# Optimization experiments

Measured on AMD Instinct MI355X. Metric: run time of the kernel, lower is better.

## Reference

```python
import jax, jax.numpy as jnp
import numpy as np

NUM_HEADS = 20


def _rope(t, pos):
    """Rotary embedding (ESM style, rotate_half on full head_dim).
    t: (T, h, d), pos: (T,) float32 position within each sequence."""
    d = t.shape[-1]
    inv_freq = 1.0 / (10000.0 ** (jnp.arange(0, d, 2, dtype=jnp.float32) / d))  # (d/2,)
    freqs = pos[:, None] * inv_freq[None, :]          # (T, d/2)
    emb = jnp.concatenate([freqs, freqs], axis=-1)    # (T, d)
    cos = jnp.cos(emb)[:, None, :]                    # (T, 1, d)
    sin = jnp.sin(emb)[:, None, :]
    x1, x2 = jnp.split(t, 2, axis=-1)
    rot = jnp.concatenate([-x2, x1], axis=-1)
    return t * cos + rot * sin


def setup_inputs() -> dict:
    key = jax.random.key(0)
    ks = jax.random.split(key, 8)
    E = 1280
    lengths = np.array([512, 768, 1024, 1024, 1024, 1280, 1280, 1280], dtype=np.int64)
    cu_lens = jnp.asarray(np.concatenate([[0], np.cumsum(lengths)]).astype(np.int32))
    T = int(lengths.sum())  # 8192
    s = (2.0 / (E + E)) ** 0.5  # xavier-ish scale
    return {
        "x": jax.random.normal(ks[0], (T, E), jnp.float32),
        "cu_lens": cu_lens,
        "max_len": 1280,
        "Wq": jax.random.normal(ks[1], (E, E), jnp.float32) * s,
        "bq": jnp.zeros((E,), jnp.float32),
        "Wk": jax.random.normal(ks[2], (E, E), jnp.float32) * s,
        "bk": jnp.zeros((E,), jnp.float32),
        "Wv": jax.random.normal(ks[3], (E, E), jnp.float32) * s,
        "bv": jnp.zeros((E,), jnp.float32),
        "Wo": jax.random.normal(ks[4], (E, E), jnp.float32) * (2.0 ** 0.5) * s,
        "bo": jnp.zeros((E,), jnp.float32),
    }


def reference(x, cu_lens, max_len, Wq, bq, Wk, bk, Wv, bv, Wo, bo):
    T, E = x.shape
    h = NUM_HEADS
    d = E // h
    scale = d ** -0.5
    # fused QKV projections (q pre-scaled, softmax_scale=1 as in the original)
    q = ((x @ Wq.T + bq) * scale).reshape(T, h, d)
    k = (x @ Wk.T + bk).reshape(T, h, d)
    v = (x @ Wv.T + bv).reshape(T, h, d)
    # per-token sequence id and within-sequence position from cu_lens
    t_idx = jnp.arange(T)
    seq_id = jnp.searchsorted(cu_lens, t_idx, side='right') - 1  # (T,)
    pos = t_idx - cu_lens[seq_id]                                # (T,) int
    # rotary on q and k with per-sequence positions
    posf = pos.astype(jnp.float32)
    q = _rope(q, posf)
    k = _rope(k, posf)
    # scatter packed tokens into padded (B, max_len, h, d) layout
    B = cu_lens.shape[0] - 1
    qp = jnp.zeros((B, max_len, h, d), q.dtype).at[seq_id, pos].set(q)
    kp = jnp.zeros((B, max_len, h, d), k.dtype).at[seq_id, pos].set(k)
    vp = jnp.zeros((B, max_len, h, d), v.dtype).at[seq_id, pos].set(v)
    valid = jnp.zeros((B, max_len), bool).at[seq_id, pos].set(True)
    # non-causal attention within each sequence (block-diagonal over packed tokens)
    scores = jnp.einsum('blhd,bmhd->bhlm', qp, kp)
    scores = jnp.where(valid[:, None, None, :], scores, -1e9)
    attn = jax.nn.softmax(scores, axis=-1)
    o = jnp.einsum('bhlm,bmhd->blhd', attn, vp)
    # gather back to packed layout and apply output projection
    out_tok = o[seq_id, pos].reshape(T, E)
    return out_tok @ Wo.T + bo
```

## Files before the change

kernel.cpp:

```cpp
#include <hip/hip_runtime.h>
#include <hip/hip_bf16.h>
#include <cstdint>

#define E_DIM   1280
#define NHEADS  20
#define HDIM    64
#define QKV_LD  3840

typedef __attribute__((ext_vector_type(8))) short bf8_t;
typedef __attribute__((ext_vector_type(4))) short bf4_t;
typedef __attribute__((ext_vector_type(4))) float f4_t;

__device__ __forceinline__ short f2bs(float f) {
    union { __hip_bfloat16 h; short s; } u;
    u.h = __float2bfloat16(f);
    return u.s;
}

__device__ __forceinline__ f4_t mfma16x32(bf8_t a, bf8_t b, f4_t c) {
    return __builtin_amdgcn_mfma_f32_16x16x32_bf16(a, b, c, 0, 0, 0);
}
__device__ __forceinline__ f4_t mfma16x16(bf4_t a, bf4_t b, f4_t c) {
    return __builtin_amdgcn_mfma_f32_16x16x16bf16_1k(a, b, c, 0, 0, 0);
}

__device__ __forceinline__ void gl_lds16(const void* g, void* l) {
    auto gp = reinterpret_cast<__attribute__((address_space(1))) unsigned int*>(
        reinterpret_cast<uintptr_t>(g));
    auto lp = reinterpret_cast<__attribute__((address_space(3))) unsigned int*>(
        reinterpret_cast<uintptr_t>(l));
    __builtin_amdgcn_global_load_lds(gp, lp, 16, 0, 0);
}

#define QSCALE 0.18033688011112042f

__device__ __forceinline__ void cvt8(__hip_bfloat16* dst, const float* src, float sc) {
    float4 a = *(const float4*)src;
    float4 b = *(const float4*)(src + 4);
    bf8_t v;
    v[0] = f2bs(a.x * sc); v[1] = f2bs(a.y * sc); v[2] = f2bs(a.z * sc); v[3] = f2bs(a.w * sc);
    v[4] = f2bs(b.x * sc); v[5] = f2bs(b.y * sc); v[6] = f2bs(b.z * sc); v[7] = f2bs(b.w * sc);
    *(bf8_t*)dst = v;
}

__global__ __launch_bounds__(256) void prep_kernel(
    const float* __restrict__ x,
    const float* __restrict__ wq, const float* __restrict__ wk,
    const float* __restrict__ wv, const float* __restrict__ wo,
    const float* __restrict__ bq, const float* __restrict__ bk, const float* __restrict__ bv,
    __hip_bfloat16* __restrict__ xbf, __hip_bfloat16* __restrict__ wqkv,
    __hip_bfloat16* __restrict__ wobf, float* __restrict__ bqkv,
    long nx8, long nw8, long nb8)
{
    long u = (long)blockIdx.x * 256 + threadIdx.x;
    if (u < nx8) { cvt8(xbf + u * 8, x + u * 8, 1.0f); return; }
    u -= nx8;
    if (u < 3 * nw8) {
        long e = u * 8;
        long w1 = nw8 * 8;
        const float* src; float sc;
        if (e < w1)            { src = wq + e;           sc = QSCALE; }
        else if (e < 2 * w1)   { src = wk + (e - w1);    sc = 1.0f; }
        else                   { src = wv + (e - 2*w1);  sc = 1.0f; }
        cvt8(wqkv + e, src, sc);
        return;
    }
    u -= 3 * nw8;
    if (u < nw8) { cvt8(wobf + u * 8, wo + u * 8, 1.0f); return; }
    u -= nw8;
    if (u < nb8) {
        long e = u * 8;
        #pragma unroll
        for (int j = 0; j < 8; j++) {
            long i = e + j;
            float v;
            if (i < E_DIM)           v = bq[i] * QSCALE;
            else if (i < 2 * E_DIM)  v = bk[i - E_DIM];
            else                     v = bv[i - 2 * E_DIM];
            bqkv[i] = v;
        }
    }
}

template<bool BF16_OUT>
__global__ __launch_bounds__(256, 3) void gemm_nt(
    const __hip_bfloat16* __restrict__ A, const __hip_bfloat16* __restrict__ Bw,
    const float* __restrict__ bias, void* __restrict__ Cout,
    int M, int N, int K, int ldc)
{
    __shared__ __align__(16) __hip_bfloat16 As[128 * 32];
    __shared__ __align__(16) __hip_bfloat16 Bs[128 * 32];
    const int t = threadIdx.x;
    const int wv = t >> 6;
    const int ln = t & 63;
    const int m16 = ln & 15, q4 = ln >> 4;
    const int row0 = blockIdx.y * 128, col0 = blockIdx.x * 128;
    const int wm = (wv >> 1) * 64, wn = (wv & 1) * 64;

    f4_t acc[4][4] = {};

    for (int k0 = 0; k0 < K; k0 += 32) {
        #pragma unroll
        for (int i = 0; i < 2; i++) {
            int s = i * 256 + t;
            int r = s >> 2, c = s & 3;
            gl_lds16(A + (size_t)(row0 + r) * K + k0 + c * 8,
                     As + (size_t)(i * 256 + wv * 64) * 8);
        }
        #pragma unroll
        for (int i = 0; i < 2; i++) {
            int s = i * 256 + t;
            int r = s >> 2, c = s & 3;
            gl_lds16(Bw + (size_t)(col0 + r) * K + k0 + c * 8,
                     Bs + (size_t)(i * 256 + wv * 64) * 8);
        }
        __syncthreads();
        bf8_t af[4], bfr[4];
        #pragma unroll
        for (int mt = 0; mt < 4; mt++)
            af[mt] = *(const bf8_t*)&As[(wm + mt * 16 + m16) * 32 + q4 * 8];
        #pragma unroll
        for (int nt = 0; nt < 4; nt++)
            bfr[nt] = *(const bf8_t*)&Bs[(wn + nt * 16 + m16) * 32 + q4 * 8];
        #pragma unroll
        for (int mt = 0; mt < 4; mt++)
            #pragma unroll
            for (int nt = 0; nt < 4; nt++)
                acc[mt][nt] = mfma16x32(af[mt], bfr[nt], acc[mt][nt]);
        __syncthreads();
    }

    #pragma unroll
    for (int nt = 0; nt < 4; nt++) {
        int cg = col0 + wn + nt * 16 + m16;
        float bv = bias[cg];
        #pragma unroll
        for (int mt = 0; mt < 4; mt++) {
            #pragma unroll
            for (int r = 0; r < 4; r++) {
                int rg = row0 + wm + mt * 16 + q4 * 4 + r;
                float v = acc[mt][nt][r] + bv;
                if constexpr (BF16_OUT)
                    ((__hip_bfloat16*)Cout)[(long)rg * ldc + cg] = __float2bfloat16(v);
                else
                    ((float*)Cout)[(long)rg * ldc + cg] = v;
            }
        }
    }
}

__global__ __launch_bounds__(256) void rope_kernel(
    __hip_bfloat16* __restrict__ qkv, const int* __restrict__ cu, int B, int T)
{
    long idx = (long)blockIdx.x * 256 + threadIdx.x;
    int i = idx & 31;
    long r = idx >> 5;
    int h = (int)(r % NHEADS);
    int tok = (int)(r / NHEADS);
    if (tok >= T) return;
    int pos = tok;
    for (int b = 1; b <= B; b++) if (tok >= cu[b]) pos = tok - cu[b];
    float f = (float)pos * exp2f(-(float)i * 0.41524100558003436f);
    float s, c;
    sincosf(f, &s, &c);
    long base = (long)tok * QKV_LD + h * HDIM + i;
    {
        float q1 = __bfloat162float(qkv[base]);
        float q2 = __bfloat162float(qkv[base + 32]);
        qkv[base]      = __float2bfloat16(q1 * c - q2 * s);
        qkv[base + 32] = __float2bfloat16(q2 * c + q1 * s);
    }
    {
        long kb = base + E_DIM;
        float k1 = __bfloat162float(qkv[kb]);
        float k2 = __bfloat162float(qkv[kb + 32]);
        qkv[kb]      = __float2bfloat16(k1 * c - k2 * s);
        qkv[kb + 32] = __float2bfloat16(k2 * c + k1 * s);
    }
}

__global__ __launch_bounds__(256) void vtrans_kernel(
    const __hip_bfloat16* __restrict__ qkv, __hip_bfloat16* __restrict__ vt, int T)
{
    long u = (long)blockIdx.x * 256 + threadIdx.x;
    int tchunks = T >> 3;
    int tc = (int)(u % tchunks);
    int hd = (int)(u / tchunks);
    if (hd >= E_DIM) return;
    long t0 = (long)tc * 8;
    bf8_t v;
    #pragma unroll
    for (int j = 0; j < 8; j++)
        v[j] = *(const short*)&qkv[(t0 + j) * QKV_LD + 2 * E_DIM + hd];
    *(bf8_t*)&vt[(long)hd * T + t0] = v;
}

__global__ __launch_bounds__(256, 2) void attn_kernel(
    const __hip_bfloat16* __restrict__ qkv, const __hip_bfloat16* __restrict__ vt,
    const int* __restrict__ cu, __hip_bfloat16* __restrict__ obuf, int B, int T)
{
    __shared__ __align__(16) __hip_bfloat16 Ks[2][128 * 64];
    __shared__ __align__(16) __hip_bfloat16 Vs[2][64 * 128];

    int idx = blockIdx.x;
    int h = idx % NHEADS;
    int gt = idx / NHEADS;
    int b = 0, l = 0, seq0 = 0;
    for (; b < B; ++b) {
        seq0 = cu[b];
        l = cu[b + 1] - seq0;
        int ntile = (l + 127) >> 7;
        if (gt < ntile) break;
        gt -= ntile;
    }
    if (b == B) return;
    int q0 = gt * 128;

    const int t = threadIdx.x;
    const int wv = t >> 6, ln = t & 63;
    const int m16 = ln & 15, q4 = ln >> 4;

    auto stage_full = [&](int kv0n, int bi) {
        #pragma unroll
        for (int i = 0; i < 4; i++) {
            int s2 = i * 256 + t;
            int key = s2 >> 3, cg = (s2 & 7) ^ (key & 7);
            gl_lds16(qkv + (long)(seq0 + kv0n + key) * QKV_LD + E_DIM + h * HDIM + cg * 8,
                     (char*)&Ks[bi][0] + (size_t)(i * 256 + wv * 64) * 16);
        }
        #pragma unroll
        for (int i = 0; i < 4; i++) {
            int s2 = i * 256 + t;
            int d = s2 >> 4, cg = (s2 & 15) ^ (d & 15);
            gl_lds16(vt + (long)(h * HDIM + d) * T + seq0 + kv0n + cg * 8,
                     (char*)&Vs[bi][0] + (size_t)(i * 256 + wv * 64) * 16);
        }
    };
    auto stage_tail = [&](int kv0n, int bi) {
        #pragma unroll
        for (int i = 0; i < 4; i++) {
            int s2 = i * 256 + t;
            int key = s2 >> 3, c = s2 & 7;
            bf8_t v = (bf8_t)0;
            if (kv0n + key < l)
                v = *(const bf8_t*)(qkv + (long)(seq0 + kv0n + key) * QKV_LD + E_DIM + h * HDIM + c * 8);
            *(bf8_t*)&Ks[bi][key * 64 + (c ^ (key & 7)) * 8] = v;
        }
        #pragma unroll
        for (int i = 0; i < 4; i++) {
            int s2 = i * 256 + t;
            int d = s2 >> 4, c = s2 & 15;
            bf8_t v = (bf8_t)0;
            int tb = kv0n + c * 8;
            #pragma unroll
            for (int u = 0; u < 8; u++)
                if (tb + u < l)
                    v[u] = *(const short*)&vt[(long)(h * HDIM + d) * T + seq0 + tb + u];
            *(bf8_t*)&Vs[bi][d * 128 + (c ^ (d & 15)) * 8] = v;
        }
    };

    if (128 <= l) stage_full(0, 0); else stage_tail(0, 0);

    bf8_t bq[2][2];
    #pragma unroll
    for (int nt = 0; nt < 2; nt++) {
        int qrow = q0 + wv * 32 + nt * 16 + m16;
        #pragma unroll
        for (int kc = 0; kc < 2; kc++) {
            bf8_t v = (bf8_t)0;
            if (qrow < l)
                v = *(const bf8_t*)(qkv + (long)(seq0 + qrow) * QKV_LD + h * HDIM + kc * 32 + q4 * 8);
            bq[nt][kc] = v;
        }
    }

    f4_t oacc[2][4] = {};
    float m_s[2] = {-1e30f, -1e30f};
    float l_s[2] = {0.0f, 0.0f};

    const int ksw0 = (q4 ^ (m16 & 7)) * 8;
    const int ksw1 = ((4 + q4) ^ (m16 & 7)) * 8;

    asm volatile("s_waitcnt vmcnt(0) lgkmcnt(0)" ::: "memory");
    __builtin_amdgcn_s_barrier();

    int cur = 0;
    for (int kv0 = 0; kv0 < l; kv0 += 128) {
        const bool full = (kv0 + 128 <= l);
        const int kvn = kv0 + 128;
        const bool has_next = kvn < l;
        if (has_next) {
            if (kvn + 128 <= l) stage_full(kvn, cur ^ 1);
            else stage_tail(kvn, cur ^ 1);
        }

        const __hip_bfloat16* Kb = Ks[cur];
        const __hip_bfloat16* Vb = Vs[cur];

        f4_t S[2][8];
        __builtin_amdgcn_s_setprio(1);
        #pragma unroll
        for (int mt = 0; mt < 8; mt++) {
            const __hip_bfloat16* krow = &Kb[(mt * 16 + m16) * 64];
            bf8_t ak0 = *(const bf8_t*)(krow + ksw0);
            bf8_t ak1 = *(const bf8_t*)(krow + ksw1);
            #pragma unroll
            for (int nt = 0; nt < 2; nt++) {
                f4_t a = {};
                a = mfma16x32(ak0, bq[nt][0], a);
                a = mfma16x32(ak1, bq[nt][1], a);
                S[nt][mt] = a;
            }
        }
        __builtin_amdgcn_s_setprio(0);

        if (!full) {
            #pragma unroll
            for (int mt = 0; mt < 8; mt++) {
                #pragma unroll
                for (int r = 0; r < 4; r++) {
                    bool valid = (kv0 + mt * 16 + q4 * 4 + r) < l;
                    #pragma unroll
                    for (int nt = 0; nt < 2; nt++)
                        if (!valid) S[nt][mt][r] = -1e30f;
                }
            }
        }

        #pragma unroll
        for (int nt = 0; nt < 2; nt++) {
            float mx = -1e30f;
            #pragma unroll
            for (int mt = 0; mt < 8; mt++)
                #pragma unroll
                for (int r = 0; r < 4; r++)
                    mx = fmaxf(mx, S[nt][mt][r]);
            mx = fmaxf(mx, __shfl_xor(mx, 16));
            mx = fmaxf(mx, __shfl_xor(mx, 32));
            if (!__all(mx - m_s[nt] <= 8.0f)) {
                float mn = fmaxf(m_s[nt], mx);
                float al = exp2f(m_s[nt] - mn);
                m_s[nt] = mn;
                l_s[nt] *= al;
                #pragma unroll
                for (int dt = 0; dt < 4; dt++)
                    #pragma unroll
                    for (int r = 0; r < 4; r++)
                        oacc[nt][dt][r] *= al;
            }
            float mcur = m_s[nt];
            float ls = 0.0f;
            #pragma unroll
            for (int mt = 0; mt < 8; mt++) {
                #pragma unroll
                for (int r = 0; r < 4; r++) {
                    float p = exp2f(S[nt][mt][r] - mcur);
                    ls += p;
                    S[nt][mt][r] = p;
                }
            }
            l_s[nt] += ls;
        }

        __builtin_amdgcn_s_setprio(1);
        #pragma unroll
        for (int mt = 0; mt < 8; mt++) {
            bf4_t bp[2];
            #pragma unroll
            for (int nt = 0; nt < 2; nt++) {
                bf4_t p;
                p[0] = f2bs(S[nt][mt][0]); p[1] = f2bs(S[nt][mt][1]);
                p[2] = f2bs(S[nt][mt][2]); p[3] = f2bs(S[nt][mt][3]);
                bp[nt] = p;
            }
            const int vsw = ((mt * 2 + (q4 >> 1)) ^ m16) * 8 + (q4 & 1) * 4;
            #pragma unroll
            for (int dt = 0; dt < 4; dt++) {
                bf4_t av = *(const bf4_t*)&Vb[(dt * 16 + m16) * 128 + vsw];
                #pragma unroll
                for (int nt = 0; nt < 2; nt++)
                    oacc[nt][dt] = mfma16x16(av, bp[nt], oacc[nt][dt]);
            }
        }
        __builtin_amdgcn_s_setprio(0);

        if (has_next) {
            asm volatile("s_waitcnt vmcnt(0) lgkmcnt(0)" ::: "memory");
            __builtin_amdgcn_s_barrier();
            cur ^= 1;
        }
    }

    #pragma unroll
    for (int nt = 0; nt < 2; nt++) {
        float ls = l_s[nt];
        ls += __shfl_xor(ls, 16);
        ls += __shfl_xor(ls, 32);
        float inv = 1.0f / ls;
        int qrow = q0 + wv * 32 + nt * 16 + m16;
        if (qrow < l) {
            #pragma unroll
            for (int dt = 0; dt < 4; dt++) {
                bf4_t o;
                #pragma unroll
                for (int r = 0; r < 4; r++)
                    o[r] = f2bs(oacc[nt][dt][r] * inv);
                *(bf4_t*)&obuf[(long)(seq0 + qrow) * E_DIM + h * HDIM + dt * 16 + q4 * 4] = o;
            }
        }
    }
}

extern "C" void kernel_launch(void* const* d_in, const int* in_sizes, int n_in,
                              void* d_out, int out_size, void* d_ws, size_t ws_size,
                              hipStream_t stream) {
    const int E = E_DIM;
    const int T = in_sizes[0] / E;
    const int B = in_sizes[1] - 1;

    const float* x  = (const float*)d_in[0];
    const int*   cu = (const int*)d_in[1];
    const float* Wq = (const float*)d_in[3];
    const float* bq = (const float*)d_in[4];
    const float* Wk = (const float*)d_in[5];
    const float* bk = (const float*)d_in[6];
    const float* Wv = (const float*)d_in[7];
    const float* bv = (const float*)d_in[8];
    const float* Wo = (const float*)d_in[9];
    const float* bo = (const float*)d_in[10];

    char* ws = (char*)d_ws;
    size_t off = 0;
    auto alloc = [&](size_t bytes) -> void* {
        void* p = ws + off;
        off = (off + bytes + 255) & ~(size_t)255;
        return p;
    };
    __hip_bfloat16* xbf   = (__hip_bfloat16*)alloc((size_t)T * E * 2);
    __hip_bfloat16* wqkv  = (__hip_bfloat16*)alloc((size_t)3 * E * E * 2);
    __hip_bfloat16* wobf  = (__hip_bfloat16*)alloc((size_t)E * E * 2);
    float*          bqkv  = (float*)alloc((size_t)3 * E * 4);
    __hip_bfloat16* qkvb  = (__hip_bfloat16*)alloc((size_t)T * 3 * E * 2);
    __hip_bfloat16* vt    = (__hip_bfloat16*)alloc((size_t)E * T * 2);
    __hip_bfloat16* obuf  = xbf;

    long nx8 = (long)T * E / 8;
    long nw8 = (long)E * E / 8;
    long nb8 = (long)3 * E / 8;
    long total = nx8 + 4 * nw8 + nb8;
    int pblocks = (int)((total + 255) / 256);
    prep_kernel<<<pblocks, 256, 0, stream>>>(x, Wq, Wk, Wv, Wo, bq, bk, bv,
                                             xbf, wqkv, wobf, bqkv, nx8, nw8, nb8);

    gemm_nt<true><<<dim3(3 * E / 128, T / 128), 256, 0, stream>>>(
        xbf, wqkv, bqkv, qkvb, T, 3 * E, E, 3 * E);

    rope_kernel<<<(int)(((long)T * NHEADS * 32) / 256), 256, 0, stream>>>(qkvb, cu, B, T);

    vtrans_kernel<<<(int)(((long)E * T / 8 + 255) / 256), 256, 0, stream>>>(qkvb, vt, T);

    int qtiles_ub = T / 128 + B;
    attn_kernel<<<qtiles_ub * NHEADS, 256, 0, stream>>>(qkvb, vt, cu, obuf, B, T);

    gemm_nt<false><<<dim3(E / 128, T / 128), 256, 0, stream>>>(
        obuf, wobf, bo, d_out, T, E, E, E);
}
```

Measured before the change: 448.9 us.

## Use 256x256-tile double-buffered GEMM with XCD swizzle for QKV projection

Adds a new GEMM kernel with 256x256 output tiles, 512 threads, double-buffered LDS staged through direct global-to-LDS loads with an XOR swizzle, s_setprio around MFMA bursts, and a block-id remap that groups workgroups by XCD. It replaces the 128x128 GEMM for the fused QKV projection only. The aim is more data reuse per tile and overlap of loads with compute. The cost is 128 KB of LDS per block, heavy register use, and a coarse grid of 32x15=480 blocks, which raises wave-quantization and occupancy risk.

```diff
diff --git a/kernel.cpp b/kernel.cpp
--- a/kernel.cpp
+++ b/kernel.cpp
@@ -149,6 +149,159 @@
     }
 }
 
+template<bool BF16_OUT>
+__global__ __launch_bounds__(512, 2) void gemm256(
+    const __hip_bfloat16* __restrict__ A, const __hip_bfloat16* __restrict__ Bw,
+    const float* __restrict__ bias, void* __restrict__ Cout,
+    int M, int N, int K, int ldc)
+{
+    __shared__ __align__(16) __hip_bfloat16 As[2][256 * 64];
+    __shared__ __align__(16) __hip_bfloat16 Bs[2][256 * 64];
+
+    const int t = threadIdx.x;
+    const int wv = t >> 6, ln = t & 63;
+    const int m16 = ln & 15, q4 = ln >> 4;
+    const int wr = wv >> 2, wc = wv & 3;
+
+    const int gx = N >> 8;
+    const int nwg = gridDim.x;
+    const int id = blockIdx.x;
+    const int swz = ((nwg & 7) == 0) ? (id & 7) * (nwg >> 3) + (id >> 3) : id;
+    const int col0 = (swz % gx) << 8;
+    const int row0 = (swz / gx) << 8;
+
+    const int NT = K >> 6;
+
+    auto stage = [&](const __hip_bfloat16* src, __hip_bfloat16* dst) {
+        #pragma unroll
+        for (int i = 0; i < 4; i++) {
+            int s = i * 512 + t;
+            int r = s >> 3, c = (s & 7) ^ (r & 7);
+            gl_lds16(src + (size_t)r * K + c * 8,
+                     (char*)dst + (size_t)(i * 512 + wv * 64) * 16);
+        }
+    };
+
+    stage(A  + (size_t)row0 * K,      &As[0][0]);
+    stage(Bw + (size_t)col0 * K,      &Bs[0][0]);
+    if (NT > 1) {
+        stage(A  + (size_t)row0 * K + 64, &As[1][0]);
+        stage(Bw + (size_t)col0 * K + 64, &Bs[1][0]);
+        asm volatile("s_waitcnt vmcnt(8)" ::: "memory");
+    } else {
+        asm volatile("s_waitcnt vmcnt(0)" ::: "memory");
+    }
+    __builtin_amdgcn_s_barrier();
+
+    f4_t acc[8][4] = {};
+
+    for (int kt = 0; kt < NT; kt++) {
+        const __hip_bfloat16* Ab = &As[kt & 1][0];
+        const __hip_bfloat16* Bb = &Bs[kt & 1][0];
+
+        auto lda = [&](const __hip_bfloat16* base, int r, int kc) {
+            return *(const bf8_t*)&base[r * 64 + ((((kc << 2) | q4) ^ (r & 7)) << 3)];
+        };
+
+        bf8_t afr[4][2], bf0[2][2], bf1[2][2];
+        #pragma unroll
+        for (int mt = 0; mt < 4; mt++)
+            #pragma unroll
+            for (int kc = 0; kc < 2; kc++)
+                afr[mt][kc] = lda(Ab, wr * 128 + mt * 16 + m16, kc);
+        #pragma unroll
+        for (int nt = 0; nt < 2; nt++)
+            #pragma unroll
+            for (int kc = 0; kc < 2; kc++)
+                bf0[nt][kc] = lda(Bb, wc * 64 + nt * 16 + m16, kc);
+
+        __builtin_amdgcn_s_setprio(1);
+        #pragma unroll
+        for (int mt = 0; mt < 4; mt++)
+            #pragma unroll
+            for (int nt = 0; nt < 2; nt++)
+                #pragma unroll
+                for (int kc = 0; kc < 2; kc++)
+                    acc[mt][nt] = mfma16x32(afr[mt][kc], bf0[nt][kc], acc[mt][nt]);
+        __builtin_amdgcn_s_setprio(0);
+
+        #pragma unroll
+        for (int nt = 0; nt < 2; nt++)
+            #pragma unroll
+            for (int kc = 0; kc < 2; kc++)
+                bf1[nt][kc] = lda(Bb, wc * 64 + (2 + nt) * 16 + m16, kc);
+
+        __builtin_amdgcn_s_setprio(1);
+        #pragma unroll
+        for (int mt = 0; mt < 4; mt++)
+            #pragma unroll
+            for (int nt = 0; nt < 2; nt++)
+                #pragma unroll
+                for (int kc = 0; kc < 2; kc++)
+                    acc[mt][2 + nt] = mfma16x32(afr[mt][kc], bf1[nt][kc], acc[mt][2 + nt]);
+        __builtin_amdgcn_s_setprio(0);
+
+        #pragma unroll
+        for (int mt = 0; mt < 4; mt++)
+            #pragma unroll
+            for (int kc = 0; kc < 2; kc++)
+                afr[mt][kc] = lda(Ab, wr * 128 + (4 + mt) * 16 + m16, kc);
+
+        __builtin_amdgcn_s_setprio(1);
+        #pragma unroll
+        for (int mt = 0; mt < 4; mt++)
+            #pragma unroll
+            for (int nt = 0; nt < 2; nt++)
+                #pragma unroll
+                for (int kc = 0; kc < 2; kc++)
+                    acc[4 + mt][2 + nt] = mfma16x32(afr[mt][kc], bf1[nt][kc], acc[4 + mt][2 + nt]);
+        __builtin_amdgcn_s_setprio(0);
+
+        __builtin_amdgcn_s_setprio(1);
+        #pragma unroll
+        for (int mt = 0; mt < 4; mt++)
+            #pragma unroll
+            for (int nt = 0; nt < 2; nt++)
+                #pragma unroll
+                for (int kc = 0; kc < 2; kc++)
+                    acc[4 + mt][nt] = mfma16x32(afr[mt][kc], bf0[nt][kc], acc[4 + mt][nt]);
+        __builtin_amdgcn_s_setprio(0);
+
+        asm volatile("s_waitcnt lgkmcnt(0)" ::: "memory");
+        __builtin_amdgcn_s_barrier();
+
+        if (kt + 2 < NT) {
+            stage(A  + (size_t)row0 * K + (size_t)(kt + 2) * 64, &As[kt & 1][0]);
+            stage(Bw + (size_t)col0 * K + (size_t)(kt + 2) * 64, &Bs[kt & 1][0]);
+        }
+        if (kt + 1 < NT) {
+            if (kt + 2 < NT)
+                asm volatile("s_waitcnt vmcnt(8)" ::: "memory");
+            else
+                asm volatile("s_waitcnt vmcnt(0)" ::: "memory");
+            __builtin_amdgcn_s_barrier();
+        }
+    }
+
+    #pragma unroll
+    for (int nt = 0; nt < 4; nt++) {
+        int cg = col0 + wc * 64 + nt * 16 + m16;
+        float bval = bias[cg];
+        #pragma unroll
+        for (int mt = 0; mt < 8; mt++) {
+            #pragma unroll
+            for (int r = 0; r < 4; r++) {
+                int rg = row0 + wr * 128 + mt * 16 + q4 * 4 + r;
+                float v = acc[mt][nt][r] + bval;
+                if constexpr (BF16_OUT)
+                    ((__hip_bfloat16*)Cout)[(long)rg * ldc + cg] = __float2bfloat16(v);
+                else
+                    ((float*)Cout)[(long)rg * ldc + cg] = v;
+            }
+        }
+    }
+}
+
 __global__ __launch_bounds__(256) void rope_kernel(
     __hip_bfloat16* __restrict__ qkv, const int* __restrict__ cu, int B, int T)
 {
@@ -453,7 +606,7 @@
     prep_kernel<<<pblocks, 256, 0, stream>>>(x, Wq, Wk, Wv, Wo, bq, bk, bv,
                                              xbf, wqkv, wobf, bqkv, nx8, nw8, nb8);
 
-    gemm_nt<true><<<dim3(3 * E / 128, T / 128), 256, 0, stream>>>(
+    gemm256<true><<<(T / 256) * (3 * E / 256), 512, 0, stream>>>(
         xbf, wqkv, bqkv, qkvb, T, 3 * E, E, 3 * E);
 
     rope_kernel<<<(int)(((long)T * NHEADS * 32) / 256), 256, 0, stream>>>(qkvb, cu, B, T);
```

New measurement: 428.0 us. 4.6% less time.
